# Optimization experiments

Hardware: AMD Instinct MI355X
Metric: run time of the kernel (lower is better)

## Reference

```python
import jax, jax.numpy as jnp
import numpy as np

GROUPSIZE = 128
# 6 possible 2:4 sparsity patterns (choose 2 nonzeros out of each group of 4 rows)
_PATTERNS = jnp.array([
    [1, 1, 0, 0], [1, 0, 1, 0], [1, 0, 0, 1],
    [0, 1, 1, 0], [0, 1, 0, 1], [0, 0, 1, 1],
], dtype=jnp.float32)


def setup_inputs() -> dict:
    key = jax.random.key(0)
    k1, k2, k3, k4 = jax.random.split(key, 4)
    M, K, N = 4096, 4096, 8192
    x = jax.random.normal(k1, (M, K), dtype=jnp.float16)
    # int4 codes in [0, 15] (stored unpacked; bit-packing is layout-only)
    qweight = jax.random.randint(k2, (K, N), 0, 16, dtype=jnp.int32)
    # 2:4 pattern index per group of 4 consecutive K rows
    meta = jax.random.randint(k3, (K // 4, N), 0, 6, dtype=jnp.int32)
    # positive group scales, typical quantization magnitude
    scale = (jax.random.uniform(k4, (K // GROUPSIZE, N), dtype=jnp.float32) * 0.02 + 0.005).astype(jnp.float16)
    return {"x": x, "qweight": qweweight_fix(qweight), "meta": meta, "scale": scale}


def qweweight_fix(q):
    return q  # identity; kept for clarity


def _dequant(qweight, meta, scale):
    """Dequantize int4 2:4-sparse weights with group scales -> dense fp32 [K, N]."""
    K, N = qweight.shape
    mask = _PATTERNS[meta]                      # [K//4, N, 4]
    mask = jnp.transpose(mask, (0, 2, 1)).reshape(K, N)  # [K, N]
    s = jnp.repeat(scale.astype(jnp.float32), GROUPSIZE, axis=0)  # [K, N]
    # symmetric int4: zero-point = 8 (maxq+1)//2
    return (qweight.astype(jnp.float32) - 8.0) * mask * s


def reference(x, qweight, meta, scale):
    W = _dequant(qweight, meta, scale)          # [K, N] fp32
    out = x.astype(jnp.float32) @ W             # fp32 accumulation, as in the kernel
    return out.astype(x.dtype)                  # [M, N] fp16
```

## Files before the change

kernel.cpp:

```cpp
#include <hip/hip_runtime.h>
#include <cmath>


typedef __attribute__((ext_vector_type(8))) short bf16x8;
typedef __attribute__((ext_vector_type(4))) float f32x4;

__device__ inline unsigned short f2bf(float f) {
    union { float f; unsigned u; } v; v.f = f;
    unsigned r = (v.u + 0x7FFFu + ((v.u >> 16) & 1u)) >> 16;
    return (unsigned short)r;
}

__global__ __launch_bounds__(256) void dequant_conv(
    const int* __restrict__ q, const int* __restrict__ meta,
    const float* __restrict__ scale,
    unsigned short* __restrict__ wt,
    const float* __restrict__ x, unsigned short* __restrict__ xb,
    long long total, int gyD,
    int K, int N, int nbase)
{
    __shared__ __align__(16) unsigned short lds[64 * 64];
    const int t = threadIdx.x;

    if ((int)blockIdx.y >= gyD) {
        const long long cid = (long long)((int)blockIdx.y - gyD) * gridDim.x
                            + blockIdx.x;
        const long long base = (cid * 256 + t) * 8;
        if (base + 8 > total) return;
        const float4 a = *reinterpret_cast<const float4*>(x + base);
        const float4 b = *reinterpret_cast<const float4*>(x + base + 4);
        uint4 o;
        o.x = (unsigned)f2bf(a.x) | ((unsigned)f2bf(a.y) << 16);
        o.y = (unsigned)f2bf(a.z) | ((unsigned)f2bf(a.w) << 16);
        o.z = (unsigned)f2bf(b.x) | ((unsigned)f2bf(b.y) << 16);
        o.w = (unsigned)f2bf(b.z) | ((unsigned)f2bf(b.w) << 16);
        *reinterpret_cast<uint4*>(xb + base) = o;
        return;
    }

    const int nlane = t & 15;
    const int kc    = t >> 4;
    const int k0    = blockIdx.x * 64;
    const int nl0   = blockIdx.y * 64;
    const int g     = k0 >> 7;
    const int kbase = k0 + kc * 4;
    const unsigned lut = 0xCA6953u;

    #pragma unroll
    for (int nn = 0; nn < 4; ++nn) {
        const int r  = nlane + nn * 16;
        const int ng = nbase + nl0 + r;
        const float sc = scale[(size_t)g * N + ng];
        const int mv = meta[(size_t)(kbase >> 2) * N + ng];
        const unsigned pat = (lut >> (mv * 4)) & 0xFu;
        unsigned short w[4];
        #pragma unroll
        for (int j = 0; j < 4; ++j) {
            const int qv = q[(size_t)(kbase + j) * N + ng];
            const float wf = ((pat >> j) & 1u) ? (float)(qv - 8) * sc : 0.0f;
            w[j] = f2bf(wf);
        }
        uint2 pk;
        pk.x = (unsigned)w[0] | ((unsigned)w[1] << 16);
        pk.y = (unsigned)w[2] | ((unsigned)w[3] << 16);
        const int off = r * 64 + ((((kc >> 1) ^ (r & 7)) << 3) | ((kc & 1) << 2));
        *reinterpret_cast<uint2*>(&lds[off]) = pk;
    }
    __syncthreads();
    #pragma unroll
    for (int p = 0; p < 2; ++p) {
        const int idx = p * 256 + t;
        const int nr  = idx >> 3;
        const int ch  = idx & 7;
        const uint4 vv = *reinterpret_cast<const uint4*>(
            &lds[nr * 64 + ((ch ^ (nr & 7)) << 3)]);
        *reinterpret_cast<uint4*>(&wt[(size_t)(nl0 + nr) * K + k0 + ch * 8]) = vv;
    }
}

#define BAR() do { asm volatile("" ::: "memory"); \
                   __builtin_amdgcn_s_barrier(); \
                   asm volatile("" ::: "memory"); } while (0)

#define GLDS(g, s) __builtin_amdgcn_global_load_lds( \
    (const __attribute__((address_space(1))) void*)(g), \
    (__attribute__((address_space(3))) void*)(s), 16, 0, 0)

#define MFMA(d, x, y) d = __builtin_amdgcn_mfma_f32_16x16x32_bf16(x, y, d, 0, 0, 0)

__global__ __launch_bounds__(512, 2) void gemm256(
    const unsigned short* __restrict__ A,
    const unsigned short* __restrict__ Bt,
    float* __restrict__ C,
    int M, int N, int K, int nbase, int mbase)
{
    __shared__ __align__(16) unsigned short As[32768];
    __shared__ __align__(16) unsigned short Bs[32768];

    const int t    = threadIdx.x;
    const int w    = t >> 6;
    const int lane = t & 63;
    const int wm   = w >> 2;
    const int wn   = w & 3;
    const int l16  = lane & 15;
    const int quad = lane >> 4;

    const int gx = gridDim.x, gy = gridDim.y;
    int bid = blockIdx.y * gx + blockIdx.x;
    const int nwg = gx * gy;
    int m0, n0;
    if ((nwg & 7) == 0 && (gy & 1) == 0 && (gx & 3) == 0) {
        const int xcd = bid & 7;
        const int idx = bid >> 3;
        const int cpr = gx >> 2;
        const int lr  = idx / cpr;
        const int lc  = idx - lr * cpr;
        m0 = ((xcd >> 2) * (gy >> 1) + lr) * 256;
        n0 = ((xcd & 3) * cpr + lc) * 256;
    } else {
        int b2 = bid;
        if (nwg >= 8) {
            const int q8 = nwg >> 3, r8 = nwg & 7;
            const int xcd = bid & 7, off = bid >> 3;
            b2 = (xcd < r8 ? xcd * (q8 + 1) : r8 * (q8 + 1) + (xcd - r8) * q8) + off;
        }
        n0 = (b2 % gx) * 256;
        m0 = (b2 / gx) * 256;
    }
    m0 += mbase;

    const int    csrc = ((lane & 7) ^ ((lane >> 3) & 7)) * 8;
    const size_t aB = (size_t)(m0 + w * 8 + (lane >> 3)) * K + csrc;
    const size_t bB = (size_t)(n0 + w * 8 + (lane >> 3)) * K + csrc;
    const size_t J  = (size_t)64 * K;
    const size_t H  = (size_t)128 * K;
    const int sdst  = w * 512;

    const int sw0 = ((quad ^ (lane & 7)) * 8);
    const int sw1 = (((4 + quad) ^ (lane & 7)) * 8);
    const int aR  = wm * 8192 + l16 * 64;
    const int bR  = (wn >> 1) * 8192 + ((wn & 1) * 64 + l16) * 64;

    int kA = 0, kB = 0;

#define STAGE_A(buf, h) do { \
    GLDS(A + aB + (size_t)(h) * H + kA, &As[(buf)*16384 + (h)*8192 + sdst]); \
    GLDS(A + aB + (size_t)(h) * H + J + kA, &As[(buf)*16384 + (h)*8192 + 4096 + sdst]); \
  } while (0)
#define STAGE_B(buf, h) do { \
    GLDS(Bt + bB + (size_t)(h) * H + kB, &Bs[(buf)*16384 + (h)*8192 + sdst]); \
    GLDS(Bt + bB + (size_t)(h) * H + J + kB, &Bs[(buf)*16384 + (h)*8192 + 4096 + sdst]); \
  } while (0)

    f32x4 acc[8][4];
    #pragma unroll
    for (int i = 0; i < 8; ++i)
        #pragma unroll
        for (int j = 0; j < 4; ++j)
            acc[i][j] = (f32x4){0.f, 0.f, 0.f, 0.f};

    STAGE_A(0, 0); STAGE_A(0, 1); kA += 64;
    STAGE_B(0, 0); STAGE_B(0, 1); kB += 64;
    STAGE_B(1, 0); STAGE_B(1, 1); kB += 64;
    asm volatile("s_waitcnt vmcnt(4)" ::: "memory");
    BAR();

    bf16x8 a[4][2], bA_[2][2], bB_[2][2];

    #pragma unroll
    for (int j = 0; j < 2; ++j) {
        bA_[j][0] = *(const bf16x8*)&Bs[bR + j * 1024 + sw0];
        bA_[j][1] = *(const bf16x8*)&Bs[bR + j * 1024 + sw1];
    }

#define PHASES(buf, obuf, bcur, bnxt) do { \
  _Pragma("unroll") for (int i = 0; i < 4; ++i) { \
    a[i][0] = *(const bf16x8*)&As[(buf)*16384 + aR + i*1024 + sw0]; \
    a[i][1] = *(const bf16x8*)&As[(buf)*16384 + aR + i*1024 + sw1]; } \
  STAGE_A(obuf, 0); \
  BAR(); \
  asm volatile("s_waitcnt lgkmcnt(0)" ::: "memory"); \
  __builtin_amdgcn_s_setprio(1); \
  _Pragma("unroll") for (int i = 0; i < 4; ++i) \
    _Pragma("unroll") for (int j = 0; j < 2; ++j) { \
      MFMA(acc[i][j], a[i][0], bcur[j][0]); MFMA(acc[i][j], a[i][1], bcur[j][1]); } \
  __builtin_amdgcn_s_setprio(0); \
  BAR(); \
  _Pragma("unroll") for (int j = 0; j < 2; ++j) { \
    bnxt[j][0] = *(const bf16x8*)&Bs[(buf)*16384 + bR + (2+j)*1024 + sw0]; \
    bnxt[j][1] = *(const bf16x8*)&Bs[(buf)*16384 + bR + (2+j)*1024 + sw1]; } \
  STAGE_A(obuf, 1); kA += 64; if (kA >= K) kA = 0; \
  BAR(); \
  asm volatile("s_waitcnt lgkmcnt(0)" ::: "memory"); \
  __builtin_amdgcn_s_setprio(1); \
  _Pragma("unroll") for (int i = 0; i < 4; ++i) \
    _Pragma("unroll") for (int j = 0; j < 2; ++j) { \
      MFMA(acc[i][2+j], a[i][0], bnxt[j][0]); MFMA(acc[i][2+j], a[i][1], bnxt[j][1]); } \
  __builtin_amdgcn_s_setprio(0); \
  BAR(); \
  _Pragma("unroll") for (int i = 0; i < 4; ++i) { \
    a[i][0] = *(const bf16x8*)&As[(buf)*16384 + aR + (4+i)*1024 + sw0]; \
    a[i][1] = *(const bf16x8*)&As[(buf)*16384 + aR + (4+i)*1024 + sw1]; } \
  STAGE_B(buf, 0); \
  BAR(); \
  asm volatile("s_waitcnt lgkmcnt(0)" ::: "memory"); \
  __builtin_amdgcn_s_setprio(1); \
  _Pragma("unroll") for (int i = 0; i < 4; ++i) \
    _Pragma("unroll") for (int j = 0; j < 2; ++j) { \
      MFMA(acc[4+i][2+j], a[i][0], bnxt[j][0]); MFMA(acc[4+i][2+j], a[i][1], bnxt[j][1]); } \
  __builtin_amdgcn_s_setprio(0); \
  asm volatile("s_waitcnt vmcnt(6)" ::: "memory"); \
  BAR(); \
  _Pragma("unroll") for (int j = 0; j < 2; ++j) { \
    bnxt[j][0] = *(const bf16x8*)&Bs[(obuf)*16384 + bR + j*1024 + sw0]; \
    bnxt[j][1] = *(const bf16x8*)&Bs[(obuf)*16384 + bR + j*1024 + sw1]; } \
  STAGE_B(buf, 1); kB += 64; if (kB >= K) kB = 0; \
  BAR(); \
  asm volatile("s_waitcnt lgkmcnt(0)" ::: "memory"); \
  __builtin_amdgcn_s_setprio(1); \
  _Pragma("unroll") for (int i = 0; i < 4; ++i) \
    _Pragma("unroll") for (int j = 0; j < 2; ++j) { \
      MFMA(acc[4+i][j], a[i][0], bcur[j][0]); MFMA(acc[4+i][j], a[i][1], bcur[j][1]); } \
  __builtin_amdgcn_s_setprio(0); \
  asm volatile("s_waitcnt vmcnt(4)" ::: "memory"); \
  BAR(); \
} while (0)

    const int NIT = K >> 7;
    for (int it = 0; it < NIT; ++it) {
        PHASES(0, 1, bA_, bB_);
        PHASES(1, 0, bB_, bA_);
    }

    asm volatile("s_waitcnt vmcnt(0)" ::: "memory");

    const int mBase = m0 + wm * 128;
    const int nBase = nbase + n0 + wn * 64;
    #pragma unroll
    for (int i = 0; i < 8; ++i) {
        const int mrow = mBase + i * 16 + quad * 4;
        #pragma unroll
        for (int j = 0; j < 4; ++j) {
            const int ncol = nBase + j * 16 + l16;
            #pragma unroll
            for (int r = 0; r < 4; ++r)
                C[(size_t)(mrow + r) * N + ncol] = acc[i][j][r];
        }
    }
#undef STAGE_A
#undef STAGE_B
#undef PHASES
}

extern "C" void kernel_launch(void* const* d_in, const int* in_sizes, int n_in,
                              void* d_out, int out_size, void* d_ws, size_t ws_size,
                              hipStream_t stream)
{
    const float* x     = (const float*)d_in[0];
    const int*   q     = (const int*)d_in[1];
    const int*   meta  = (const int*)d_in[2];
    const float* scale = (const float*)d_in[3];
    float*       out   = (float*)d_out;

    const double s0 = (double)in_sizes[0];
    const double s1 = (double)in_sizes[1];
    const int K = (int)llround(sqrt(s0 * s1 / (double)out_size));
    const int M = in_sizes[0] / K;
    const int N = in_sizes[1] / K;

    unsigned short* xb = (unsigned short*)d_ws;
    const size_t xb_bytes = (size_t)M * (size_t)K * 2;
    unsigned short* wt = (unsigned short*)((char*)d_ws + xb_bytes);
    const size_t wt_avail = ws_size > xb_bytes ? ws_size - xb_bytes : 0;

    const long long total = (long long)M * K;
    long long maxrows = (long long)(wt_avail / ((size_t)K * 2));
    int NC = (int)((maxrows / 256) * 256);
    if (NC > N) NC = N;
    if (NC < 256) NC = 256;

    const int gxD = K / 64;
    const long long conv_blocks = (total / 8 + 255) / 256;

    for (int nbase = 0; nbase < N; nbase += NC) {
        const int nc = (N - nbase) < NC ? (N - nbase) : NC;
        const int gyD = nc / 64;
        const int gyC = (nbase == 0)
            ? (int)((conv_blocks + gxD - 1) / gxD) : 0;
        dim3 g1(gxD, gyD + gyC);
        dequant_conv<<<g1, dim3(256), 0, stream>>>(
            q, meta, scale, wt, x, xb, total, gyD, K, N, nbase);
        const int Mh = M / 2;
        for (int h = 0; h < 2; ++h) {
            dim3 g2(nc / 256, Mh / 256);
            gemm256<<<g2, dim3(512), 0, stream>>>(
                xb, wt, out, M, N, K, nbase, h * Mh);
        }
    }
}
```

Before: 566.9 us.

## Vectorize and pipeline dequant loads, nontemporal stores, merge GEMM halves into one launch

```diff
diff --git a/kernel.cpp b/kernel.cpp
--- a/kernel.cpp
+++ b/kernel.cpp
@@ -4,6 +4,7 @@
 
 typedef __attribute__((ext_vector_type(8))) short bf16x8;
 typedef __attribute__((ext_vector_type(4))) float f32x4;
+typedef __attribute__((ext_vector_type(4))) unsigned int u32x4;
 
 __device__ inline unsigned short f2bf(float f) {
     union { float f; unsigned u; } v; v.f = f;
@@ -25,57 +26,82 @@
     if ((int)blockIdx.y >= gyD) {
         const long long cid = (long long)((int)blockIdx.y - gyD) * gridDim.x
                             + blockIdx.x;
-        const long long base = (cid * 256 + t) * 8;
-        if (base + 8 > total) return;
-        const float4 a = *reinterpret_cast<const float4*>(x + base);
-        const float4 b = *reinterpret_cast<const float4*>(x + base + 4);
-        uint4 o;
-        o.x = (unsigned)f2bf(a.x) | ((unsigned)f2bf(a.y) << 16);
-        o.y = (unsigned)f2bf(a.z) | ((unsigned)f2bf(a.w) << 16);
-        o.z = (unsigned)f2bf(b.x) | ((unsigned)f2bf(b.y) << 16);
-        o.w = (unsigned)f2bf(b.z) | ((unsigned)f2bf(b.w) << 16);
-        *reinterpret_cast<uint4*>(xb + base) = o;
+        const long long bbase = cid * 8192;
+        #pragma unroll
+        for (int j = 0; j < 4; ++j) {
+            const long long base = bbase + (long long)j * 2048 + (long long)t * 8;
+            if (base + 8 > total) return;
+            const float4 a = *reinterpret_cast<const float4*>(x + base);
+            const float4 b = *reinterpret_cast<const float4*>(x + base + 4);
+            u32x4 o;
+            o.x = (unsigned)f2bf(a.x) | ((unsigned)f2bf(a.y) << 16);
+            o.y = (unsigned)f2bf(a.z) | ((unsigned)f2bf(a.w) << 16);
+            o.z = (unsigned)f2bf(b.x) | ((unsigned)f2bf(b.y) << 16);
+            o.w = (unsigned)f2bf(b.z) | ((unsigned)f2bf(b.w) << 16);
+            __builtin_nontemporal_store(o, reinterpret_cast<u32x4*>(xb + base));
+        }
         return;
     }
 
-    const int nlane = t & 15;
-    const int kc    = t >> 4;
-    const int k0    = blockIdx.x * 64;
-    const int nl0   = blockIdx.y * 64;
-    const int g     = k0 >> 7;
-    const int kbase = k0 + kc * 4;
+    const int l    = t & 15;
+    const int kc   = t >> 4;
+    const int n4   = l * 4;
+    const int k0   = blockIdx.x * 256;
+    const int nl0  = blockIdx.y * 64;
+    const int ng   = nbase + nl0 + n4;
     const unsigned lut = 0xCA6953u;
+    const int slot = ((kc >> 1) ^ l) & 7;
+    const int woff = (slot << 3) | ((kc & 1) << 2);
+
+    int4   q4[2][4];
+    int4   mv4[2];
+    float4 sc4[2];
+
+#define DQLOAD(ph, s) do { \
+    const int kb = k0 + (s) * 64 + kc * 4; \
+    sc4[ph] = *reinterpret_cast<const float4*>(&scale[(size_t)((k0 + (s)*64) >> 7) * N + ng]); \
+    mv4[ph] = *reinterpret_cast<const int4*>(&meta[(size_t)(kb >> 2) * N + ng]); \
+    _Pragma("unroll") for (int j = 0; j < 4; ++j) \
+        q4[ph][j] = *reinterpret_cast<const int4*>(&q[(size_t)(kb + j) * N + ng]); \
+  } while (0)
+
+    DQLOAD(0, 0);
 
     #pragma unroll
-    for (int nn = 0; nn < 4; ++nn) {
-        const int r  = nlane + nn * 16;
-        const int ng = nbase + nl0 + r;
-        const float sc = scale[(size_t)g * N + ng];
-        const int mv = meta[(size_t)(kbase >> 2) * N + ng];
-        const unsigned pat = (lut >> (mv * 4)) & 0xFu;
-        unsigned short w[4];
-        #pragma unroll
-        for (int j = 0; j < 4; ++j) {
-            const int qv = q[(size_t)(kbase + j) * N + ng];
-            const float wf = ((pat >> j) & 1u) ? (float)(qv - 8) * sc : 0.0f;
-            w[j] = f2bf(wf);
-        }
-        uint2 pk;
-        pk.x = (unsigned)w[0] | ((unsigned)w[1] << 16);
-        pk.y = (unsigned)w[2] | ((unsigned)w[3] << 16);
-        const int off = r * 64 + ((((kc >> 1) ^ (r & 7)) << 3) | ((kc & 1) << 2));
-        *reinterpret_cast<uint2*>(&lds[off]) = pk;
-    }
-    __syncthreads();
-    #pragma unroll
-    for (int p = 0; p < 2; ++p) {
-        const int idx = p * 256 + t;
-        const int nr  = idx >> 3;
-        const int ch  = idx & 7;
-        const uint4 vv = *reinterpret_cast<const uint4*>(
-            &lds[nr * 64 + ((ch ^ (nr & 7)) << 3)]);
-        *reinterpret_cast<uint4*>(&wt[(size_t)(nl0 + nr) * K + k0 + ch * 8]) = vv;
-    }
+    for (int s = 0; s < 4; ++s) {
+        const int ph = s & 1;
+        #pragma unroll
+        for (int nn = 0; nn < 4; ++nn) {
+            const int mv = ((const int*)&mv4[ph])[nn];
+            const unsigned pat = (lut >> (mv * 4)) & 0xFu;
+            const float sc = ((const float*)&sc4[ph])[nn];
+            unsigned short w[4];
+            #pragma unroll
+            for (int j = 0; j < 4; ++j) {
+                const int qv = ((const int*)&q4[ph][j])[nn];
+                const float wf = ((pat >> j) & 1u) ? (float)(qv - 8) * sc : 0.0f;
+                w[j] = f2bf(wf);
+            }
+            uint2 pk;
+            pk.x = (unsigned)w[0] | ((unsigned)w[1] << 16);
+            pk.y = (unsigned)w[2] | ((unsigned)w[3] << 16);
+            *reinterpret_cast<uint2*>(&lds[(n4 + nn) * 64 + woff]) = pk;
+        }
+        if (s < 3) DQLOAD(ph ^ 1, s + 1);
+        __syncthreads();
+        #pragma unroll
+        for (int p = 0; p < 2; ++p) {
+            const int idx = p * 256 + t;
+            const int nr  = idx >> 3;
+            const int ch  = idx & 7;
+            const u32x4 vv = *reinterpret_cast<const u32x4*>(
+                &lds[nr * 64 + (((ch ^ (nr >> 2)) & 7) << 3)]);
+            __builtin_nontemporal_store(vv, reinterpret_cast<u32x4*>(
+                &wt[(size_t)(nl0 + nr) * K + k0 + s * 64 + ch * 8]));
+        }
+        if (s < 3) __syncthreads();
+    }
+#undef DQLOAD
 }
 
 #define BAR() do { asm volatile("" ::: "memory"); \
@@ -92,7 +118,7 @@
     const unsigned short* __restrict__ A,
     const unsigned short* __restrict__ Bt,
     float* __restrict__ C,
-    int M, int N, int K, int nbase, int mbase)
+    int M, int N, int K, int nbase)
 {
     __shared__ __align__(16) unsigned short As[32768];
     __shared__ __align__(16) unsigned short Bs[32768];
@@ -127,7 +153,6 @@
         n0 = (b2 % gx) * 256;
         m0 = (b2 / gx) * 256;
     }
-    m0 += mbase;
 
     const int    csrc = ((lane & 7) ^ ((lane >> 3) & 7)) * 8;
     const size_t aB = (size_t)(m0 + w * 8 + (lane >> 3)) * K + csrc;
@@ -279,8 +304,8 @@
     if (NC > N) NC = N;
     if (NC < 256) NC = 256;
 
-    const int gxD = K / 64;
-    const long long conv_blocks = (total / 8 + 255) / 256;
+    const int gxD = K / 256;
+    const long long conv_blocks = (total + 8191) / 8192;
 
     for (int nbase = 0; nbase < N; nbase += NC) {
         const int nc = (N - nbase) < NC ? (N - nbase) : NC;
@@ -290,11 +315,7 @@
         dim3 g1(gxD, gyD + gyC);
         dequant_conv<<<g1, dim3(256), 0, stream>>>(
             q, meta, scale, wt, x, xb, total, gyD, K, N, nbase);
-        const int Mh = M / 2;
-        for (int h = 0; h < 2; ++h) {
-            dim3 g2(nc / 256, Mh / 256);
-            gemm256<<<g2, dim3(512), 0, stream>>>(
-                xb, wt, out, M, N, K, nbase, h * Mh);
-        }
+        dim3 g2(nc / 256, M / 256);
+        gemm256<<<g2, dim3(512), 0, stream>>>(xb, wt, out, M, N, K, nbase);
     }
 }
```

New measurement: 584.9 us. 3.2% more time.
